# Performance work log

Measured on AMD Instinct MI355X. Metric: run time of the kernel, lower is better.

## Reference

```python
import jax, jax.numpy as jnp
import numpy as np

B, L, H, N = 256, 50, 128, 100000
NEG_MASK = -1.0e9  # value used by torch masked_fill_ on attention scores


def setup_inputs() -> dict:
    key = jax.random.key(0)
    ks = jax.random.split(key, 12)
    s = 1.0 / np.sqrt(H)
    return {
        "all_memory": jax.random.normal(ks[0], (B, L, H), jnp.float32),
        "last_memory": jax.random.normal(ks[1], (B, H), jnp.float32),
        "seq_item": jax.random.randint(ks[2], (B, L), 0, N),
        "mask": jnp.zeros((B, L), dtype=bool),
        # parameters (eval mode: dropout is identity)
        "Ue_w": jax.random.normal(ks[3], (H, H), jnp.float32) * s,
        "Ue_b": jnp.zeros((H,), jnp.float32),
        "We_w": jax.random.normal(ks[4], (H, H), jnp.float32) * s,
        "We_b": jnp.zeros((H,), jnp.float32),
        "Ve_w": jax.random.normal(ks[5], (H, 1), jnp.float32) * s,
        "Ve_b": jnp.zeros((1,), jnp.float32),
        "Wexp": jax.random.normal(ks[6], (2 * H, N), jnp.float32) * (1.0 / np.sqrt(2 * H)),
    }


def reference(all_memory, last_memory, seq_item, mask,
              Ue_w, Ue_b, We_w, We_b, Ve_w, Ve_b, Wexp):
    # Additive (Bahdanau) attention over the sequence
    a = jnp.einsum('blh,hk->blk', all_memory, Ue_w) + Ue_b          # [B,L,H]
    q = last_memory @ We_w + We_b                                    # [B,H]
    scores = jnp.squeeze(jnp.tanh(a + q[:, None, :]) @ Ve_w, -1) + Ve_b  # [B,L]
    scores = jnp.where(mask, NEG_MASK, scores)
    attn = jax.nn.softmax(scores, axis=1)                            # [B,L]
    ctx = jnp.einsum('bl,blh->bh', attn, all_memory)                 # [B,H]
    feat = jnp.concatenate([ctx, last_memory], axis=1)               # [B,2H]
    logits = feat @ Wexp                                             # [B,N]
    # explore mask: count of each item in the history (positions with item>0),
    # equivalent to bmm((seq_item>0), one_hot(seq_item)) without the dense one-hot
    valid = (seq_item > 0).astype(logits.dtype)                      # [B,L]
    counts = jnp.zeros((B, N), logits.dtype).at[
        jnp.arange(B)[:, None], seq_item].add(valid)                 # [B,N]
    logits = jnp.where(counts > 0, -jnp.inf, logits)
    return jax.nn.softmax(logits, axis=1)
```

## Files before the change

### kernel.cpp

```cpp
#include <hip/hip_runtime.h>
#include <math.h>

#define B_ 256
#define L_ 50
#define H_ 128
#define N_ 100000
#define K_ 256
#define NREP 64

typedef __attribute__((ext_vector_type(8))) short short8;
typedef __attribute__((ext_vector_type(4))) float f32x4;

__device__ inline short f2bf(float x) {
  union { float f; unsigned u; } v; v.f = x;
  unsigned r = (v.u + 0x7fff + ((v.u >> 16) & 1)) >> 16;
  return (short)r;
}
__device__ inline float bf2f(short h) {
  union { unsigned u; float f; } v; v.u = ((unsigned)(unsigned short)h) << 16;
  return v.f;
}

__global__ __launch_bounds__(256)
void attn_feat_kernel(const float* __restrict__ am, const float* __restrict__ lm,
    const float* __restrict__ Ue_w, const float* __restrict__ Ue_b,
    const float* __restrict__ We_w, const float* __restrict__ We_b,
    const float* __restrict__ Ve_w, const float* __restrict__ Ve_b,
    const unsigned char* __restrict__ mask,
    short* __restrict__ feat_hi, short* __restrict__ feat_lo,
    float* __restrict__ sums_rep)
{
  const int b = blockIdx.x;
  const int t = threadIdx.x;
  __shared__ float UeS[H_ * H_];
  __shared__ float amS[L_][H_];
  __shared__ float lmS[H_], qS[H_];
  __shared__ float attnS[64];
  __shared__ float redW[4][32];

  if (t < 64) sums_rep[b * 64 + t] = 0.0f;

  for (int i = t; i < H_ * H_ / 4; i += 256)
    ((float4*)UeS)[i] = ((const float4*)Ue_w)[i];
  for (int i = t; i < L_ * H_ / 4; i += 256)
    ((float4*)amS)[i] = ((const float4*)(am + (size_t)b * L_ * H_))[i];
  if (t < H_) lmS[t] = lm[b * H_ + t];
  __syncthreads();

  if (t < H_) {
    float q = We_b[t];
    #pragma unroll 8
    for (int h = 0; h < H_; ++h) q += lmS[h] * We_w[h * H_ + t];
    qS[t] = q;
  }
  __syncthreads();

  const int k = t & 127, half = t >> 7, wv = t >> 6, lk = t & 63;
  const float ve  = Ve_w[k];
  const float ueb = Ue_b[k];
  const float veb = Ve_b[0];
  for (int li = 0; li < 25; ++li) {
    const int l = half * 25 + li;
    float a = ueb;
    #pragma unroll 8
    for (int h = 0; h < H_; ++h) a = fmaf(amS[l][h], UeS[h * H_ + k], a);
    float v = tanhf(a + qS[k]) * ve;
    #pragma unroll
    for (int off = 32; off > 0; off >>= 1) v += __shfl_down(v, off, 64);
    if (lk == 0) redW[wv][li] = v;
  }
  __syncthreads();
  if (t < 50) {
    const int hf = t / 25, li = t - hf * 25;
    attnS[t] = redW[hf * 2][li] + redW[hf * 2 + 1][li] + veb;
  }
  __syncthreads();

  if (t < 64) {
    float s = (t < L_) ? attnS[t] : -3.0e38f;
    if (t < L_ && mask[b * L_ + t]) s = -1.0e9f;
    float m = s;
    #pragma unroll
    for (int off = 32; off > 0; off >>= 1) m = fmaxf(m, __shfl_xor(m, off));
    float e = (t < L_) ? __expf(s - m) : 0.0f;
    float tot = e;
    #pragma unroll
    for (int off = 32; off > 0; off >>= 1) tot += __shfl_xor(tot, off);
    if (t < L_) attnS[t] = e / tot;
  }
  __syncthreads();

  if (t < H_) {
    float c = 0.0f;
    #pragma unroll
    for (int l = 0; l < L_; ++l) c = fmaf(attnS[l], amS[l][t], c);
    short h1 = f2bf(c);
    feat_hi[b * K_ + t] = h1;
    feat_lo[b * K_ + t] = f2bf(c - bf2f(h1));
    float lv = lmS[t];
    short h2 = f2bf(lv);
    feat_hi[b * K_ + H_ + t] = h2;
    feat_lo[b * K_ + H_ + t] = f2bf(lv - bf2f(h2));
  }
}

#define TN 64
#define KC 64

__global__ __launch_bounds__(256)
void logits_mfma_kernel(const short* __restrict__ feat_hi, const short* __restrict__ feat_lo,
                        const float* __restrict__ Wexp, float* __restrict__ out,
                        float* __restrict__ sums_rep)
{
  __shared__ __align__(16) short bhS[2][TN * KC];
  __shared__ __align__(16) short blS[2][TN * KC];

  const int t = threadIdx.x;
  const int w = t >> 6;
  const int ln = t & 15, quad = (t >> 4) & 3;
  const int n0 = blockIdx.x * TN;
  const bool tail = (n0 + TN > N_);

  const int sn  = t & 63;
  const int skb = (t >> 6) << 4;
  const int ssx = (sn & 7) << 4;

  f32x4 acc[4][4];
  #pragma unroll
  for (int i = 0; i < 4; ++i)
    #pragma unroll
    for (int j = 0; j < 4; ++j) acc[i][j] = (f32x4)(0.0f);

  float r[16];

  #define LOADC(kc_)                                                           \
    do {                                                                       \
      if (!tail) {                                                             \
        const float* g = Wexp + (size_t)((kc_) + skb) * N_ + n0 + sn;          \
        _Pragma("unroll")                                                      \
        for (int i = 0; i < 16; ++i) r[i] = g[(size_t)i * N_];                 \
      } else {                                                                 \
        const bool ok = (n0 + sn) < N_;                                        \
        const int gn = ok ? (n0 + sn) : (N_ - 1);          \
        const float* g = Wexp + (size_t)((kc_) + skb) * N_ + gn;               \
        _Pragma("unroll")                                                      \
        for (int i = 0; i < 16; ++i) { float v = g[(size_t)i * N_]; r[i] = ok ? v : 0.0f; } \
      }                                                                        \
    } while (0)

  #define CONVW(bufi)                                                          \
    do {                                                                       \
      short8 h2[2], l2[2];                                                     \
      _Pragma("unroll")                                                        \
      for (int c_ = 0; c_ < 2; ++c_) {                                         \
        _Pragma("unroll")                                                      \
        for (int j_ = 0; j_ < 8; ++j_) {                                       \
          union { float f; unsigned u; } v_; v_.f = r[c_ * 8 + j_];            \
          union { unsigned u; float f; } hv_; hv_.u = v_.u & 0xffff0000u;      \
          h2[c_][j_] = (short)(v_.u >> 16);                                    \
          l2[c_][j_] = f2bf(v_.f - hv_.f);                                     \
        }                                                                      \
      }                                                                        \
      char* ph_ = (char*)&bhS[bufi][0] + sn * 128;                             \
      char* pl_ = (char*)&blS[bufi][0] + sn * 128;                             \
      *(short8*)(ph_ + ((skb * 2)      ^ ssx)) = h2[0];                        \
      *(short8*)(ph_ + ((skb * 2 + 16) ^ ssx)) = h2[1];                        \
      *(short8*)(pl_ + ((skb * 2)      ^ ssx)) = l2[0];                        \
      *(short8*)(pl_ + ((skb * 2 + 16) ^ ssx)) = l2[1];                        \
    } while (0)

  #define LGKM_BARRIER() asm volatile("s_waitcnt lgkmcnt(0)\n\ts_barrier" ::: "memory")

  LOADC(0);
  CONVW(0);
  LOADC(KC);
  LGKM_BARRIER();

  #pragma unroll
  for (int c = 0; c < K_ / KC; ++c) {
    const int cb = c & 1;
    const int kc = c * KC;

    #pragma unroll
    for (int kk = 0; kk < KC; kk += 32) {
      short8 ah[4], al[4];
      const int kof = kc + kk + quad * 8;
      #pragma unroll
      for (int mt = 0; mt < 4; ++mt) {
        const int m = w * 64 + mt * 16 + ln;
        ah[mt] = *(const short8*)(feat_hi + m * K_ + kof);
        al[mt] = *(const short8*)(feat_lo + m * K_ + kof);
      }
      short8 bh[4], bl[4];
      #pragma unroll
      for (int nt = 0; nt < 4; ++nt) {
        const int n = nt * 16 + ln;
        const int off = (kk * 2 + quad * 16) ^ ((n & 7) << 4);
        bh[nt] = *(const short8*)((const char*)&bhS[cb][0] + n * 128 + off);
        bl[nt] = *(const short8*)((const char*)&blS[cb][0] + n * 128 + off);
      }
      #pragma unroll
      for (int mt = 0; mt < 4; ++mt)
        #pragma unroll
        for (int nt = 0; nt < 4; ++nt) {
          acc[mt][nt] = __builtin_amdgcn_mfma_f32_16x16x32_bf16(ah[mt], bh[nt], acc[mt][nt], 0, 0, 0);
          acc[mt][nt] = __builtin_amdgcn_mfma_f32_16x16x32_bf16(ah[mt], bl[nt], acc[mt][nt], 0, 0, 0);
          acc[mt][nt] = __builtin_amdgcn_mfma_f32_16x16x32_bf16(al[mt], bh[nt], acc[mt][nt], 0, 0, 0);
        }
    }

    if (c + 1 < K_ / KC) {
      CONVW((c + 1) & 1);
      if (c + 2 < K_ / KC) LOADC((c + 2) * KC);
      LGKM_BARRIER();
    }
  }

  float rs[4][4];
  #pragma unroll
  for (int mt = 0; mt < 4; ++mt)
    #pragma unroll
    for (int r_ = 0; r_ < 4; ++r_) rs[mt][r_] = 0.0f;

  #pragma unroll
  for (int mt = 0; mt < 4; ++mt) {
    #pragma unroll
    for (int nt = 0; nt < 4; ++nt) {
      const int col = n0 + nt * 16 + ln;
      #pragma unroll
      for (int r_ = 0; r_ < 4; ++r_) {
        const int row = w * 64 + mt * 16 + quad * 4 + r_;
        const float e = __expf(acc[mt][nt][r_]);
        if (col < N_) {
          out[(size_t)row * N_ + col] = e;
          rs[mt][r_] += e;
        }
      }
    }
  }
  #pragma unroll
  for (int off = 8; off > 0; off >>= 1)
    #pragma unroll
    for (int mt = 0; mt < 4; ++mt)
      #pragma unroll
      for (int r_ = 0; r_ < 4; ++r_) rs[mt][r_] += __shfl_down(rs[mt][r_], off, 16);
  if (ln == 0) {
    float* rep = sums_rep + (blockIdx.x & (NREP - 1)) * 256;
    #pragma unroll
    for (int mt = 0; mt < 4; ++mt)
      #pragma unroll
      for (int r_ = 0; r_ < 4; ++r_)
        atomicAdd(&rep[w * 64 + mt * 16 + quad * 4 + r_], rs[mt][r_]);
  }
}

__global__ __launch_bounds__(256)
void reduce_sums_kernel(const float* __restrict__ sums_rep, float* __restrict__ sums)
{
  const int b = threadIdx.x;
  float s = 0.0f;
  #pragma unroll
  for (int r = 0; r < NREP; ++r) s += sums_rep[r * 256 + b];
  sums[b] = s;
}

__global__ __launch_bounds__(256)
void mask_kernel(const int* __restrict__ seq, float* __restrict__ out, float* __restrict__ sums)
{
  int idx = blockIdx.x * 256 + threadIdx.x;
  if (idx >= B_ * L_) return;
  int b = idx / L_;
  int item = seq[idx];
  if (item > 0) {
    float old = atomicExch(&out[(size_t)b * N_ + item], 0.0f);
    if (old != 0.0f) atomicAdd(&sums[b], -old);
  }
}

#define NV4 (N_ / 4)
__global__ __launch_bounds__(256)
void norm_kernel(float* __restrict__ out, const float* __restrict__ sums)
{
  const int b = blockIdx.y;
  const float inv = 1.0f / sums[b];
  float4* row = (float4*)(out + (size_t)b * N_);
  const int i0 = blockIdx.x * (256 * 4) + threadIdx.x;
  #pragma unroll
  for (int u = 0; u < 4; ++u) {
    const int i = i0 + u * 256;
    if (i < NV4) {
      float4 v = row[i];
      v.x *= inv; v.y *= inv; v.z *= inv; v.w *= inv;
      row[i] = v;
    }
  }
}

extern "C" void kernel_launch(void* const* d_in, const int* in_sizes, int n_in,
                              void* d_out, int out_size, void* d_ws, size_t ws_size,
                              hipStream_t stream)
{
  const float* am   = (const float*)d_in[0];
  const float* lm   = (const float*)d_in[1];
  const int*   seq  = (const int*)d_in[2];
  const unsigned char* mask = (const unsigned char*)d_in[3];
  const float* Ue_w = (const float*)d_in[4];
  const float* Ue_b = (const float*)d_in[5];
  const float* We_w = (const float*)d_in[6];
  const float* We_b = (const float*)d_in[7];
  const float* Ve_w = (const float*)d_in[8];
  const float* Ve_b = (const float*)d_in[9];
  const float* Wexp = (const float*)d_in[10];
  float* out = (float*)d_out;

  short* feat_hi  = (short*)d_ws;
  short* feat_lo  = feat_hi + B_ * K_;
  float* sums_rep = (float*)(feat_lo + B_ * K_);
  float* sums     = sums_rep + NREP * 256;

  attn_feat_kernel<<<B_, 256, 0, stream>>>(am, lm, Ue_w, Ue_b, We_w, We_b,
                                           Ve_w, Ve_b, mask, feat_hi, feat_lo, sums_rep);
  logits_mfma_kernel<<<(N_ + TN - 1) / TN, 256, 0, stream>>>(feat_hi, feat_lo, Wexp, out, sums_rep);
  reduce_sums_kernel<<<1, 256, 0, stream>>>(sums_rep, sums);
  mask_kernel<<<(B_ * L_ + 255) / 256, 256, 0, stream>>>(seq, out, sums);
  dim3 gN((NV4 + 256 * 4 - 1) / (256 * 4), B_);
  norm_kernel<<<gN, 256, 0, stream>>>(out, sums);
}
```

Before: 368.9 us.

## Process two N-tiles per block with continuous Wexp prefetch pipeline

The logits GEMM kernel now launches 782 blocks, and each handles up to two 64-column tiles. The Wexp load and bf16-split pipeline runs straight across the tile boundary, so the prefetch for the second tile overlaps the first tile's compute and epilogue. The row-sum reduction is also reworked: after an extra cross-lane shuffle step, each lane issues a single atomicAdd instead of only the 16-lane leaders issuing 16 atomics each. The cost is a runtime-bounded loop that is no longer fully unrolled, and fewer blocks in flight, which lowers the parallelism available to hide memory latency.

New measurement: 371.0 us. No clear change (+0.6%).

```diff
diff --git a/kernel.cpp b/kernel.cpp
--- a/kernel.cpp
+++ b/kernel.cpp
@@ -106,6 +106,8 @@
 
 #define TN 64
 #define KC 64
+#define NTILES ((N_ + TN - 1) / TN)
+#define PBLOCKS 782
 
 __global__ __launch_bounds__(256)
 void logits_mfma_kernel(const short* __restrict__ feat_hi, const short* __restrict__ feat_lo,
@@ -117,9 +119,15 @@
 
   const int t = threadIdx.x;
   const int w = t >> 6;
+  const int lane = t & 63;
   const int ln = t & 15, quad = (t >> 4) & 3;
-  const int n0 = blockIdx.x * TN;
-  const bool tail = (n0 + TN > N_);
+
+  const int tile0 = blockIdx.x;
+  const int tile1 = blockIdx.x + PBLOCKS;
+  const int total = (tile1 < NTILES) ? 8 : 4;
+
+  #define CHUNK_N0(j_) ((((j_) < 4) ? tile0 : tile1) * TN)
+  #define CHUNK_KC(j_) (((j_) & 3) * KC)
 
   const int sn  = t & 63;
   const int skb = (t >> 6) << 4;
@@ -131,20 +139,22 @@
     #pragma unroll
     for (int j = 0; j < 4; ++j) acc[i][j] = (f32x4)(0.0f);
 
-  float r[16];
-
-  #define LOADC(kc_)                                                           \
+  float rg[16];
+
+  #define LOADC(j_)                                                            \
     do {                                                                       \
-      if (!tail) {                                                             \
-        const float* g = Wexp + (size_t)((kc_) + skb) * N_ + n0 + sn;          \
+      const int n0_ = CHUNK_N0(j_);                                            \
+      const int kc_ = CHUNK_KC(j_);                                            \
+      if (n0_ + TN <= N_) {                                                    \
+        const float* g = Wexp + (size_t)(kc_ + skb) * N_ + n0_ + sn;           \
         _Pragma("unroll")                                                      \
-        for (int i = 0; i < 16; ++i) r[i] = g[(size_t)i * N_];                 \
+        for (int i = 0; i < 16; ++i) rg[i] = g[(size_t)i * N_];                \
       } else {                                                                 \
-        const bool ok = (n0 + sn) < N_;                                        \
-        const int gn = ok ? (n0 + sn) : (N_ - 1);          \
-        const float* g = Wexp + (size_t)((kc_) + skb) * N_ + gn;               \
+        const bool ok = (n0_ + sn) < N_;                                       \
+        const int gn = ok ? (n0_ + sn) : (N_ - 1);         \
+        const float* g = Wexp + (size_t)(kc_ + skb) * N_ + gn;                 \
         _Pragma("unroll")                                                      \
-        for (int i = 0; i < 16; ++i) { float v = g[(size_t)i * N_]; r[i] = ok ? v : 0.0f; } \
+        for (int i = 0; i < 16; ++i) { float v = g[(size_t)i * N_]; rg[i] = ok ? v : 0.0f; } \
       }                                                                        \
     } while (0)
 
@@ -155,7 +165,7 @@
       for (int c_ = 0; c_ < 2; ++c_) {                                         \
         _Pragma("unroll")                                                      \
         for (int j_ = 0; j_ < 8; ++j_) {                                       \
-          union { float f; unsigned u; } v_; v_.f = r[c_ * 8 + j_];            \
+          union { float f; unsigned u; } v_; v_.f = rg[c_ * 8 + j_];           \
           union { unsigned u; float f; } hv_; hv_.u = v_.u & 0xffff0000u;      \
           h2[c_][j_] = (short)(v_.u >> 16);                                    \
           l2[c_][j_] = f2bf(v_.f - hv_.f);                                     \
@@ -173,13 +183,12 @@
 
   LOADC(0);
   CONVW(0);
-  LOADC(KC);
+  LOADC(1);
   LGKM_BARRIER();
 
-  #pragma unroll
-  for (int c = 0; c < K_ / KC; ++c) {
-    const int cb = c & 1;
-    const int kc = c * KC;
+  for (int j = 0; j < total; ++j) {
+    const int cb = j & 1;
+    const int kc = CHUNK_KC(j);
 
     #pragma unroll
     for (int kk = 0; kk < KC; kk += 32) {
@@ -209,48 +218,60 @@
         }
     }
 
-    if (c + 1 < K_ / KC) {
-      CONVW((c + 1) & 1);
-      if (c + 2 < K_ / KC) LOADC((c + 2) * KC);
+    if (j + 1 < total) {
+      CONVW((j + 1) & 1);
+      if (j + 2 < total) LOADC(j + 2);
       LGKM_BARRIER();
     }
-  }
-
-  float rs[4][4];
-  #pragma unroll
-  for (int mt = 0; mt < 4; ++mt)
-    #pragma unroll
-    for (int r_ = 0; r_ < 4; ++r_) rs[mt][r_] = 0.0f;
-
-  #pragma unroll
-  for (int mt = 0; mt < 4; ++mt) {
-    #pragma unroll
-    for (int nt = 0; nt < 4; ++nt) {
-      const int col = n0 + nt * 16 + ln;
-      #pragma unroll
-      for (int r_ = 0; r_ < 4; ++r_) {
-        const int row = w * 64 + mt * 16 + quad * 4 + r_;
-        const float e = __expf(acc[mt][nt][r_]);
-        if (col < N_) {
-          out[(size_t)row * N_ + col] = e;
-          rs[mt][r_] += e;
+
+    if ((j & 3) == 3) {
+      const int n0 = CHUNK_N0(j);
+      float rs[4][4];
+      #pragma unroll
+      for (int mt = 0; mt < 4; ++mt)
+        #pragma unroll
+        for (int r_ = 0; r_ < 4; ++r_) rs[mt][r_] = 0.0f;
+
+      #pragma unroll
+      for (int mt = 0; mt < 4; ++mt) {
+        #pragma unroll
+        for (int nt = 0; nt < 4; ++nt) {
+          const int col = n0 + nt * 16 + ln;
+          #pragma unroll
+          for (int r_ = 0; r_ < 4; ++r_) {
+            const int row = w * 64 + mt * 16 + quad * 4 + r_;
+            const float e = __expf(acc[mt][nt][r_]);
+            if (col < N_) {
+              out[(size_t)row * N_ + col] = e;
+              rs[mt][r_] += e;
+            }
+          }
         }
       }
+      #pragma unroll
+      for (int off = 8; off > 0; off >>= 1)
+        #pragma unroll
+        for (int mt = 0; mt < 4; ++mt)
+          #pragma unroll
+          for (int r_ = 0; r_ < 4; ++r_) rs[mt][r_] += __shfl_down(rs[mt][r_], off, 16);
+
+      float myrs = 0.0f;
+      const int srcl = ((lane >> 2) & 3) * 16;
+      #pragma unroll
+      for (int mt = 0; mt < 4; ++mt)
+        #pragma unroll
+        for (int r_ = 0; r_ < 4; ++r_) {
+          const float v = __shfl(rs[mt][r_], srcl, 64);
+          if ((lane >> 4) == mt && (lane & 3) == r_) myrs = v;
+        }
+      float* rep = sums_rep + (blockIdx.x & (NREP - 1)) * 256;
+      atomicAdd(&rep[w * 64 + lane], myrs);
+
+      #pragma unroll
+      for (int mt = 0; mt < 4; ++mt)
+        #pragma unroll
+        for (int nt = 0; nt < 4; ++nt) acc[mt][nt] = (f32x4)(0.0f);
     }
-  }
-  #pragma unroll
-  for (int off = 8; off > 0; off >>= 1)
-    #pragma unroll
-    for (int mt = 0; mt < 4; ++mt)
-      #pragma unroll
-      for (int r_ = 0; r_ < 4; ++r_) rs[mt][r_] += __shfl_down(rs[mt][r_], off, 16);
-  if (ln == 0) {
-    float* rep = sums_rep + (blockIdx.x & (NREP - 1)) * 256;
-    #pragma unroll
-    for (int mt = 0; mt < 4; ++mt)
-      #pragma unroll
-      for (int r_ = 0; r_ < 4; ++r_)
-        atomicAdd(&rep[w * 64 + mt * 16 + quad * 4 + r_], rs[mt][r_]);
   }
 }
 
@@ -320,7 +341,7 @@
 
   attn_feat_kernel<<<B_, 256, 0, stream>>>(am, lm, Ue_w, Ue_b, We_w, We_b,
                                            Ve_w, Ve_b, mask, feat_hi, feat_lo, sums_rep);
-  logits_mfma_kernel<<<(N_ + TN - 1) / TN, 256, 0, stream>>>(feat_hi, feat_lo, Wexp, out, sums_rep);
+  logits_mfma_kernel<<<PBLOCKS, 256, 0, stream>>>(feat_hi, feat_lo, Wexp, out, sums_rep);
   reduce_sums_kernel<<<1, 256, 0, stream>>>(sums_rep, sums);
   mask_kernel<<<(B_ * L_ + 255) / 256, 256, 0, stream>>>(seq, out, sums);
   dim3 gN((NV4 + 256 * 4 - 1) / (256 * 4), B_);
```
